# Optimization experiments

Hardware: AMD Instinct MI355X
Metric: run time of the kernel (lower is better)

## Reference

```python
import jax, jax.numpy as jnp
import numpy as np
import math

B, N, M, C, H = 8, 2048, 2048, 512, 8
DK = C // H
EPS_LN = 1e-5


def _layernorm(x, g, b):
    mu = jnp.mean(x, axis=-1, keepdims=True)
    var = jnp.var(x, axis=-1, keepdims=True)
    return (x - mu) / jnp.sqrt(var + EPS_LN) * g + b


def setup_inputs() -> dict:
    key = jax.random.key(0)
    ks = jax.random.split(key, 8)
    s = 0.02
    return {
        "cross_x": jax.random.normal(ks[0], (B, N, C), jnp.float32),
        "cross_y": jax.random.normal(ks[1], (B, M, C), jnp.float32),
        "ln_x_g": jnp.ones((C,), jnp.float32),
        "ln_x_b": jnp.zeros((C,), jnp.float32),
        "ln_y_g": jnp.ones((C,), jnp.float32),
        "ln_y_b": jnp.zeros((C,), jnp.float32),
        "Wq": jax.random.normal(ks[2], (C, C), jnp.float32) * s,
        "bq": jnp.zeros((C,), jnp.float32),
        "Wk": jax.random.normal(ks[3], (C, C), jnp.float32) * s,
        "bk": jnp.zeros((C,), jnp.float32),
        "Wv": jax.random.normal(ks[4], (C, C), jnp.float32) * s,
        "bv": jnp.zeros((C,), jnp.float32),
        "Wc": jax.random.normal(ks[5], (C, C), jnp.float32) * s,  # conv1x1 weight [out, in]
        "bc": jnp.zeros((C,), jnp.float32),
        "ln_o_g": jnp.ones((C,), jnp.float32),
        "ln_o_b": jnp.zeros((C,), jnp.float32),
    }


def reference(cross_x, cross_y, ln_x_g, ln_x_b, ln_y_g, ln_y_b,
              Wq, bq, Wk, bk, Wv, bv, Wc, bc, ln_o_g, ln_o_b):
    b, n, c = cross_x.shape
    m = cross_y.shape[1]
    xn = _layernorm(cross_x, ln_x_g, ln_x_b)
    yn = _layernorm(cross_y, ln_y_g, ln_y_b)
    # projections -> [B, H, seq, dk]
    q = (xn @ Wq + bq).reshape(b, n, H, DK).transpose(0, 2, 1, 3)
    k = (yn @ Wk + bk).reshape(b, m, H, DK).transpose(0, 2, 1, 3)
    v = (yn @ Wv + bv).reshape(b, m, H, DK).transpose(0, 2, 1, 3)
    scale = 1.0 / math.sqrt(DK)
    scores = jnp.einsum("bhnd,bhmd->bhnm", q, k) * scale
    attn = jax.nn.softmax(scores, axis=-1)
    # extra renormalization across the HEAD dimension (dim=1)
    attn = attn / (1e-9 + jnp.sum(attn, axis=1, keepdims=True))
    # dropout is identity in eval/reference mode
    o = jnp.einsum("bhnm,bhmd->bhnd", attn, v)
    q_flat = q.transpose(0, 2, 1, 3).reshape(b, n, c)  # [B, N, C]
    o_flat = o.transpose(0, 2, 1, 3).reshape(b, n, c)
    # conv1x1 over channels on (query - x)
    h = (q_flat - o_flat) @ Wc.T + bc
    h = jax.nn.leaky_relu(_layernorm(h, ln_o_g, ln_o_b), negative_slope=0.02)
    return q_flat + h
```

## Files before the change

kernel.cpp:

```cpp
#include <hip/hip_runtime.h>


typedef short bf16x8 __attribute__((ext_vector_type(8)));
typedef float f32x4 __attribute__((ext_vector_type(4)));

#define CS 0.18033688f

#define BARRIER_LG() do { __builtin_amdgcn_sched_barrier(0); \
  asm volatile("s_waitcnt lgkmcnt(0)" ::: "memory"); \
  __builtin_amdgcn_s_barrier(); \
  __builtin_amdgcn_sched_barrier(0); } while(0)

#define VMCNT(N) do { __builtin_amdgcn_sched_barrier(0); \
  asm volatile("s_waitcnt vmcnt(" #N ")" ::: "memory"); \
  __builtin_amdgcn_sched_barrier(0); } while(0)

__device__ inline float b2f(unsigned short u){
  union { unsigned int i; float f; } c; c.i = ((unsigned int)u) << 16; return c.f;
}
__device__ inline unsigned short f2b(float f){
  union { float ff; unsigned int i; } c; c.ff = f;
  unsigned int i = c.i;
  return (unsigned short)((i + 0x7FFFu + ((i >> 16) & 1u)) >> 16);
}
__device__ inline float fast_rcp(float x){ return __builtin_amdgcn_rcpf(x); }
__device__ inline f32x4 mfma16(bf16x8 a, bf16x8 b, f32x4 c){
  return __builtin_amdgcn_mfma_f32_16x16x32_bf16(a, b, c, 0, 0, 0);
}
__device__ __forceinline__ void gl16(const unsigned short* g, unsigned short* l){
  __builtin_amdgcn_global_load_lds(
      (const __attribute__((address_space(1))) unsigned int*)g,
      (__attribute__((address_space(3))) unsigned int*)l,
      16, 0, 0);
}

__global__ void detect_dtype(const unsigned int* __restrict__ g, int* __restrict__ flag){
  *flag = (g[0] == 0x3F800000u) ? 1 : 0;
}

__global__ void zero_f32(float* __restrict__ p, int n){
  int i = blockIdx.x * 256 + threadIdx.x;
  if (i < n) p[i] = 0.0f;
}

__global__ void convert_misc(const void* Wc, const void* bq, const void* bk,
    const void* bv, const void* bc, const void* go, const void* bo,
    unsigned short* WcB, unsigned short* bqB, unsigned short* bkB,
    unsigned short* bvB, unsigned short* bcB, unsigned short* goB,
    unsigned short* boB, const int* __restrict__ flag){
  int i = blockIdx.x * 256 + threadIdx.x;
  const void* src; unsigned short* dst; int o;
  if (i < 262144){ src = Wc; dst = WcB; o = i; }
  else {
    int j = i - 262144; int seg = j >> 9; o = j & 511;
    if (seg == 0){ src = bq; dst = bqB; }
    else if (seg == 1){ src = bk; dst = bkB; }
    else if (seg == 2){ src = bv; dst = bvB; }
    else if (seg == 3){ src = bc; dst = bcB; }
    else if (seg == 4){ src = go; dst = goB; }
    else if (seg == 5){ src = bo; dst = boB; }
    else return;
  }
  if (*flag) dst[o] = f2b(((const float*)src)[o]);
  else       dst[o] = ((const unsigned short*)src)[o];
}

__global__ __launch_bounds__(128) void ln_rows(const void* __restrict__ xv,
    const void* __restrict__ gxv, const void* __restrict__ bxv,
    const void* __restrict__ yv, const void* __restrict__ gyv, const void* __restrict__ byv,
    unsigned short* __restrict__ outx, unsigned short* __restrict__ outy,
    const int* __restrict__ flag){
  int row = blockIdx.x & 16383;
  int sel = blockIdx.x >> 14;
  const void* src = sel ? yv : xv;
  const void* gv = sel ? gyv : gxv;
  const void* bv_ = sel ? byv : bxv;
  unsigned short* out = sel ? outy : outx;
  int t = threadIdx.x;
  float v0, v1, v2, v3, g0, g1, g2, g3, bb0, bb1, bb2, bb3;
  if (*flag){
    float4 xf = ((const float4*)((const float*)src + (size_t)row * 512))[t];
    v0 = xf.x; v1 = xf.y; v2 = xf.z; v3 = xf.w;
    float4 gf = ((const float4*)gv)[t];  g0 = gf.x; g1 = gf.y; g2 = gf.z; g3 = gf.w;
    float4 bf = ((const float4*)bv_)[t]; bb0 = bf.x; bb1 = bf.y; bb2 = bf.z; bb3 = bf.w;
  } else {
    ushort4 raw = ((const ushort4*)((const unsigned short*)src + (size_t)row * 512))[t];
    v0 = b2f(raw.x); v1 = b2f(raw.y); v2 = b2f(raw.z); v3 = b2f(raw.w);
    ushort4 gr = ((const ushort4*)gv)[t];  g0 = b2f(gr.x); g1 = b2f(gr.y); g2 = b2f(gr.z); g3 = b2f(gr.w);
    ushort4 br = ((const ushort4*)bv_)[t]; bb0 = b2f(br.x); bb1 = b2f(br.y); bb2 = b2f(br.z); bb3 = b2f(br.w);
  }
  float s = v0 + v1 + v2 + v3;
  float sq = v0*v0 + v1*v1 + v2*v2 + v3*v3;
  #pragma unroll
  for (int off = 32; off; off >>= 1){
    s += __shfl_down(s, off, 64);
    sq += __shfl_down(sq, off, 64);
  }
  __shared__ float red[4];
  if ((t & 63) == 0){ red[(t >> 6)*2] = s; red[(t >> 6)*2 + 1] = sq; }
  __syncthreads();
  s = red[0] + red[2]; sq = red[1] + red[3];
  float mu = s * (1.0f/512.0f);
  float rstd = rsqrtf(sq * (1.0f/512.0f) - mu*mu + 1e-5f);
  ushort4 o;
  o.x = f2b((v0 - mu)*rstd*g0 + bb0);
  o.y = f2b((v1 - mu)*rstd*g1 + bb1);
  o.z = f2b((v2 - mu)*rstd*g2 + bb2);
  o.w = f2b((v3 - mu)*rstd*g3 + bb3);
  ((ushort4*)(out + (size_t)row * 512))[t] = o;
}

__global__ __launch_bounds__(256) void transposeW(const void* __restrict__ wq,
    const void* __restrict__ wk, const void* __restrict__ wv,
    unsigned short* __restrict__ oq, unsigned short* __restrict__ ok,
    unsigned short* __restrict__ ov, const int* __restrict__ flag){
  __shared__ unsigned short tile[32][33];
  const void* in = (blockIdx.z == 0) ? wq : (blockIdx.z == 1) ? wk : wv;
  unsigned short* outp = (blockIdx.z == 0) ? oq : (blockIdx.z == 1) ? ok : ov;
  int k0 = blockIdx.x * 32, j0 = blockIdx.y * 32;
  int t = threadIdx.x;
  int r = t >> 3, c4 = (t & 7) * 4;
  if (*flag){
    float4 v = *(const float4*)((const float*)in + (size_t)(k0 + r) * 512 + j0 + c4);
    tile[r][c4] = f2b(v.x); tile[r][c4+1] = f2b(v.y);
    tile[r][c4+2] = f2b(v.z); tile[r][c4+3] = f2b(v.w);
  } else {
    ushort4 v = *(const ushort4*)((const unsigned short*)in + (size_t)(k0 + r) * 512 + j0 + c4);
    tile[r][c4] = v.x; tile[r][c4+1] = v.y; tile[r][c4+2] = v.z; tile[r][c4+3] = v.w;
  }
  __syncthreads();
  ushort4 o;
  o.x = tile[c4][r]; o.y = tile[c4+1][r]; o.z = tile[c4+2][r]; o.w = tile[c4+3][r];
  *(ushort4*)(outp + (size_t)(j0 + r) * 512 + k0 + c4) = o;
}

template<int OUT_MODE>
__global__ __launch_bounds__(256) void gemm_nt(const unsigned short* __restrict__ A,
    const unsigned short* __restrict__ Bt, const unsigned short* __restrict__ bias,
    void* __restrict__ Cout){
  __shared__ __align__(16) unsigned short As[128*32];
  __shared__ __align__(16) unsigned short Bs[128*32];
  int i0 = blockIdx.x * 128;
  int j0 = blockIdx.y * 128;
  int t = threadIdx.x;
  int w = t >> 6, lane = t & 63;
  int quad = lane >> 4, l15 = lane & 15;
  int wrow = (w >> 1) * 64, wcol = (w & 1) * 64;
  f32x4 acc[4][4];
  #pragma unroll
  for (int a = 0; a < 4; a++)
    #pragma unroll
    for (int b = 0; b < 4; b++)
      acc[a][b] = (f32x4){0.f, 0.f, 0.f, 0.f};

  int ra0 = t >> 2, ca0 = (t & 3) * 8;
  const unsigned short* Ag = A + (size_t)i0 * 512;
  const unsigned short* Bg = Bt + (size_t)j0 * 512;

  for (int kt = 0; kt < 16; kt++){
    int k0 = kt * 32;
    int4 av0 = *(const int4*)(Ag + (size_t)ra0 * 512 + k0 + ca0);
    int4 av1 = *(const int4*)(Ag + (size_t)(64 + ra0) * 512 + k0 + ca0);
    int4 bv0 = *(const int4*)(Bg + (size_t)ra0 * 512 + k0 + ca0);
    int4 bv1 = *(const int4*)(Bg + (size_t)(64 + ra0) * 512 + k0 + ca0);
    __syncthreads();
    ((int4*)As)[t] = av0; ((int4*)As)[t + 256] = av1;
    ((int4*)Bs)[t] = bv0; ((int4*)Bs)[t + 256] = bv1;
    __syncthreads();
    bf16x8 af[4], bfg[4];
    #pragma unroll
    for (int a = 0; a < 4; a++)
      af[a] = *(const bf16x8*)&As[(wrow + a*16 + l15)*32 + quad*8];
    #pragma unroll
    for (int b = 0; b < 4; b++)
      bfg[b] = *(const bf16x8*)&Bs[(wcol + b*16 + l15)*32 + quad*8];
    #pragma unroll
    for (int a = 0; a < 4; a++)
      #pragma unroll
      for (int b = 0; b < 4; b++)
        acc[a][b] = mfma16(af[a], bfg[b], acc[a][b]);
  }

  #pragma unroll
  for (int b = 0; b < 4; b++){
    int gcol = j0 + wcol + b*16 + l15;
    float bv = b2f(bias[gcol]);
    #pragma unroll
    for (int a = 0; a < 4; a++){
      #pragma unroll
      for (int r = 0; r < 4; r++){
        int grow = i0 + wrow + a*16 + quad*4 + r;
        float v = acc[a][b][r] + bv;
        if (OUT_MODE == 0){
          ((unsigned short*)Cout)[(size_t)grow*512 + gcol] = f2b(v);
        } else {
          int bb_ = grow >> 11, m = grow & 2047;
          int h = gcol >> 6, d = gcol & 63;
          ((unsigned short*)Cout)[((size_t)((bb_*8 + h)*64 + d))*2048 + m] = f2b(v);
        }
      }
    }
  }
}

__global__ __launch_bounds__(256) void attn_lsum(const unsigned short* __restrict__ Qm,
    const unsigned short* __restrict__ Km, float* __restrict__ Lsum){
  int wgl = blockIdx.x * 4 + (threadIdx.x >> 6);
  int b = wgl >> 9; int r_ = wgl & 511;
  int ntl = r_ >> 4; int ms = (r_ >> 2) & 3; int hg = r_ & 3;
  int h0 = hg * 2;
  int lane = threadIdx.x & 63, quad = lane >> 4, l15 = lane & 15;
  int n0 = ntl * 64;
  const unsigned short* Kp = Km + ((size_t)(b*2048)) * 512;
  bf16x8 aq[4][2][2];
  #pragma unroll
  for (int ns = 0; ns < 4; ns++)
    #pragma unroll
    for (int hh = 0; hh < 2; hh++)
      #pragma unroll
      for (int ks = 0; ks < 2; ks++)
        aq[ns][hh][ks] = *(const bf16x8*)(Qm + ((size_t)(b*2048 + n0 + ns*16 + l15))*512
                                          + (h0+hh)*64 + ks*32 + quad*8);
  float ls[4][2];
  #pragma unroll
  for (int ns = 0; ns < 4; ns++){ ls[ns][0] = 0.f; ls[ns][1] = 0.f; }
  for (int mt = 0; mt < 16; mt++){
    int m0 = ms*512 + mt*32;
    #pragma unroll
    for (int msub = 0; msub < 2; msub++){
      int mb = m0 + msub*16;
      #pragma unroll
      for (int hh = 0; hh < 2; hh++){
        bf16x8 ak0 = *(const bf16x8*)(Kp + (size_t)(mb + l15)*512 + (h0+hh)*64 + quad*8);
        bf16x8 ak1 = *(const bf16x8*)(Kp + (size_t)(mb + l15)*512 + (h0+hh)*64 + 32 + quad*8);
        #pragma unroll
        for (int ns = 0; ns < 4; ns++){
          f32x4 S = (f32x4){0.f,0.f,0.f,0.f};
          S = mfma16(ak0, aq[ns][hh][0], S);
          S = mfma16(ak1, aq[ns][hh][1], S);
          float e0 = exp2f(S[0]*CS), e1 = exp2f(S[1]*CS);
          float e2 = exp2f(S[2]*CS), e3 = exp2f(S[3]*CS);
          ls[ns][hh] += (e0 + e1) + (e2 + e3);
        }
      }
    }
  }
  #pragma unroll
  for (int ns = 0; ns < 4; ns++)
    #pragma unroll
    for (int hh = 0; hh < 2; hh++){
      float v = ls[ns][hh];
      v += __shfl_xor(v, 16, 64);
      v += __shfl_xor(v, 32, 64);
      ls[ns][hh] = v;
    }
  if (lane < 16){
    #pragma unroll
    for (int ns = 0; ns < 4; ns++)
      #pragma unroll
      for (int hh = 0; hh < 2; hh++)
        atomicAdd(&Lsum[(size_t)(b*8 + h0 + hh)*2048 + n0 + ns*16 + lane], ls[ns][hh]);
  }
}

__global__ __launch_bounds__(1024, 4) void attn_out(const unsigned short* __restrict__ Qm,
    const unsigned short* __restrict__ Km, const unsigned short* __restrict__ VTm,
    const float* __restrict__ Lsum, unsigned short* __restrict__ DQO){
  __shared__ __align__(16) unsigned short Ks[32*512];
  __shared__ __align__(16) unsigned short Vs[512*32];
  __shared__ __align__(16) float ps[4*4*16*36];
  __shared__ __align__(16) unsigned short pbv[4*4*2*16*40];
  int bid = blockIdx.x;
  int b = bid & 7;
  int ntl = bid >> 3;
  int t = threadIdx.x;
  int w = t >> 6;
  int hp = w & 3;
  int nsub = w >> 2;
  int lane = t & 63, quad = lane >> 4, l15 = lane & 15;
  int h0 = hp * 2;
  int n0 = ntl * 64 + nsub * 16;
  int kx = (l15 & 7) << 4;

  const unsigned short* Kg = Km + (size_t)b * 1048576;
  const unsigned short* Vg = VTm + (size_t)b * 1048576;
  const unsigned short* Qp = Qm + ((size_t)(b*2048 + n0)) * 512;

  bf16x8 aq[2][2];
  #pragma unroll
  for (int hh = 0; hh < 2; hh++)
    #pragma unroll
    for (int ks = 0; ks < 2; ks++)
      aq[hh][ks] = *(const bf16x8*)(Qp + (size_t)l15*512 + (h0+hh)*64 + ks*32 + quad*8);
  float lg[2];
  #pragma unroll
  for (int hh = 0; hh < 2; hh++)
    lg[hh] = -log2f(Lsum[(size_t)(b*8 + h0 + hh)*2048 + n0 + l15]);
  f32x4 oacc[2][4];
  #pragma unroll
  for (int hh = 0; hh < 2; hh++)
    #pragma unroll
    for (int d = 0; d < 4; d++)
      oacc[hh][d] = (f32x4){0.f,0.f,0.f,0.f};

  int ksl = (lane ^ (w & 7)) << 3;
  int vro = (lane >> 2), vco = (lane & 3) * 8;
  unsigned short* kd0 = Ks + (w << 9);
  unsigned short* kd1 = Ks + ((w + 16) << 9);
  unsigned short* vd0 = Vs + (w << 9);
  unsigned short* vd1 = Vs + ((w + 16) << 9);

  float* psn = ps + nsub * 2304;
  float* pso = psn + hp * 576 + l15 * 36;
  unsigned short* pbn = pbv + nsub * 5120 + hp * 1280;

  gl16(Kg + ((size_t)(w     ) << 9) + ksl, kd0);
  gl16(Kg + ((size_t)(w + 16) << 9) + ksl, kd1);
  gl16(Vg + ((size_t)( w*16       + vro) << 11) + vco, vd0);
  gl16(Vg + ((size_t)((w+16)*16   + vro) << 11) + vco, vd1);

  for (int mt = 0; mt < 64; mt++){
    VMCNT(2);
    BARRIER_LG();
    float p[2][2][4];
    f32x4 s_own[2];
    #pragma unroll
    for (int msub = 0; msub < 2; msub++){
      const char* kr = (const char*)Ks + ((msub*16 + l15) << 10);
      #pragma unroll
      for (int hh = 0; hh < 2; hh++){
        int cb = (h0 + hh) * 128;
        bf16x8 k0 = *(const bf16x8*)(kr + ((cb + quad*16) ^ kx));
        bf16x8 k1 = *(const bf16x8*)(kr + ((cb + 64 + quad*16) ^ kx));
        f32x4 S = (f32x4){0.f,0.f,0.f,0.f};
        S = mfma16(k0, aq[hh][0], S);
        S = mfma16(k1, aq[hh][1], S);
        #pragma unroll
        for (int r = 0; r < 4; r++) p[hh][msub][r] = exp2f(fmaf(S[r], CS, lg[hh]));
      }
      f32x4 so;
      #pragma unroll
      for (int r = 0; r < 4; r++) so[r] = p[0][msub][r] + p[1][msub][r];
      s_own[msub] = so;
      *(f32x4*)(pso + msub*16 + quad*4) = so;
    }
    VMCNT(0);
    BARRIER_LG();
    if (mt < 63){
      const unsigned short* Kt = Kg + ((size_t)(mt+1) << 14);
      gl16(Kt + ((size_t)(w     ) << 9) + ksl, kd0);
      gl16(Kt + ((size_t)(w + 16) << 9) + ksl, kd1);
    }
    f32x4 ir4[2];
    #pragma unroll
    for (int msub = 0; msub < 2; msub++){
      f32x4 tt = s_own[msub];
      #pragma unroll
      for (int j = 1; j < 4; j++){
        int hq = (hp + j) & 3;
        tt += *(const f32x4*)(psn + hq*576 + l15*36 + msub*16 + quad*4);
      }
      f32x4 ir;
      #pragma unroll
      for (int r = 0; r < 4; r++) ir[r] = fast_rcp(1e-9f + tt[r]);
      ir4[msub] = ir;
    }
    #pragma unroll
    for (int hh = 0; hh < 2; hh++){
      #pragma unroll
      for (int msub = 0; msub < 2; msub++){
        unsigned int lo = (unsigned int)f2b(p[hh][msub][0]*ir4[msub][0])
                        | ((unsigned int)f2b(p[hh][msub][1]*ir4[msub][1]) << 16);
        unsigned int hi = (unsigned int)f2b(p[hh][msub][2]*ir4[msub][2])
                        | ((unsigned int)f2b(p[hh][msub][3]*ir4[msub][3]) << 16);
        int2 pv; pv.x = (int)lo; pv.y = (int)hi;
        *(int2*)&pbn[(hh*16 + l15)*40 + msub*16 + quad*4] = pv;
      }
    }
    #pragma unroll
    for (int hh = 0; hh < 2; hh++){
      bf16x8 wp = *(const bf16x8*)((const char*)pbn + (hh*16 + l15)*80 + quad*16);
      const char* vb = (const char*)Vs + (((h0+hh)*64 + l15) << 6) + quad*16;
      #pragma unroll
      for (int d = 0; d < 4; d++){
        bf16x8 vv = *(const bf16x8*)(vb + (d << 10));
        oacc[hh][d] = mfma16(vv, wp, oacc[hh][d]);
      }
    }
    BARRIER_LG();
    if (mt < 63){
      int m1 = (mt + 1) * 32;
      gl16(Vg + ((size_t)( w*16     + vro) << 11) + m1 + vco, vd0);
      gl16(Vg + ((size_t)((w+16)*16 + vro) << 11) + m1 + vco, vd1);
    }
  }
  {
    size_t nrow = (size_t)(b*2048 + n0 + l15);
    const unsigned short* Qrow = Qm + nrow * 512;
    unsigned short* Drow = DQO + nrow * 512;
    #pragma unroll
    for (int hh = 0; hh < 2; hh++){
      #pragma unroll
      for (int d = 0; d < 4; d++){
        int c = (h0+hh)*64 + d*16 + quad*4;
        ushort4 qv = *(const ushort4*)(Qrow + c);
        ushort4 ov;
        ov.x = f2b(b2f(qv.x) - oacc[hh][d][0]);
        ov.y = f2b(b2f(qv.y) - oacc[hh][d][1]);
        ov.z = f2b(b2f(qv.z) - oacc[hh][d][2]);
        ov.w = f2b(b2f(qv.w) - oacc[hh][d][3]);
        *(ushort4*)(Drow + c) = ov;
      }
    }
  }
}

__global__ __launch_bounds__(128) void finalize_k(const unsigned short* __restrict__ H,
    const unsigned short* __restrict__ Qb, const unsigned short* __restrict__ g,
    const unsigned short* __restrict__ bb, void* __restrict__ outp,
    const int* __restrict__ flag){
  int row = blockIdx.x; int t = threadIdx.x;
  ushort4 hraw = ((const ushort4*)(H + (size_t)row * 512))[t];
  float h0 = b2f(hraw.x), h1 = b2f(hraw.y), h2 = b2f(hraw.z), h3 = b2f(hraw.w);
  float s = h0 + h1 + h2 + h3;
  float sq = h0*h0 + h1*h1 + h2*h2 + h3*h3;
  #pragma unroll
  for (int off = 32; off; off >>= 1){
    s += __shfl_down(s, off, 64);
    sq += __shfl_down(sq, off, 64);
  }
  __shared__ float red[4];
  if ((t & 63) == 0){ red[(t >> 6)*2] = s; red[(t >> 6)*2 + 1] = sq; }
  __syncthreads();
  s = red[0] + red[2]; sq = red[1] + red[3];
  float mu = s * (1.0f/512.0f);
  float rstd = rsqrtf(sq * (1.0f/512.0f) - mu*mu + 1e-5f);
  ushort4 gr = ((const ushort4*)g)[t];
  ushort4 br = ((const ushort4*)bb)[t];
  ushort4 qr = ((const ushort4*)(Qb + (size_t)row * 512))[t];
  float y0 = (h0 - mu)*rstd*b2f(gr.x) + b2f(br.x); y0 = fmaxf(y0, 0.02f*y0);
  float y1 = (h1 - mu)*rstd*b2f(gr.y) + b2f(br.y); y1 = fmaxf(y1, 0.02f*y1);
  float y2 = (h2 - mu)*rstd*b2f(gr.z) + b2f(br.z); y2 = fmaxf(y2, 0.02f*y2);
  float y3 = (h3 - mu)*rstd*b2f(gr.w) + b2f(br.w); y3 = fmaxf(y3, 0.02f*y3);
  float o0 = b2f(qr.x) + y0, o1 = b2f(qr.y) + y1, o2 = b2f(qr.z) + y2, o3 = b2f(qr.w) + y3;
  if (*flag){
    float4 o; o.x = o0; o.y = o1; o.z = o2; o.w = o3;
    ((float4*)((float*)outp + (size_t)row * 512))[t] = o;
  } else {
    ushort4 o; o.x = f2b(o0); o.y = f2b(o1); o.z = f2b(o2); o.w = f2b(o3);
    ((ushort4*)((unsigned short*)outp + (size_t)row * 512))[t] = o;
  }
}

extern "C" void kernel_launch(void* const* d_in, const int* in_sizes, int n_in,
                              void* d_out, int out_size, void* d_ws, size_t ws_size,
                              hipStream_t stream){
  const void* x      = d_in[0];
  const void* y      = d_in[1];
  const void* ln_x_g = d_in[2];
  const void* ln_x_b = d_in[3];
  const void* ln_y_g = d_in[4];
  const void* ln_y_b = d_in[5];
  const void* Wq     = d_in[6];
  const void* bq     = d_in[7];
  const void* Wk     = d_in[8];
  const void* bk     = d_in[9];
  const void* Wv     = d_in[10];
  const void* bv     = d_in[11];
  const void* Wc     = d_in[12];
  const void* bc     = d_in[13];
  const void* ln_o_g = d_in[14];
  const void* ln_o_b = d_in[15];

  const size_t MB = (size_t)1 << 20;
  char* ws = (char*)d_ws;
  unsigned short* Qb  = (unsigned short*)(ws);
  unsigned short* Kb  = (unsigned short*)(ws + 16*MB);
  unsigned short* VT  = (unsigned short*)(ws + 32*MB);
  unsigned short* XN  = (unsigned short*)(ws + 48*MB);
  unsigned short* YN  = (unsigned short*)(ws + 64*MB);
  unsigned short* DQO = XN;
  unsigned short* Hpre = YN;
  unsigned short* WqT = (unsigned short*)(ws + 80*MB);
  unsigned short* WkT = WqT + 512*512;
  unsigned short* WvT = WkT + 512*512;
  unsigned short* WcB = WvT + 512*512;
  unsigned short* bqB = (unsigned short*)(ws + 82*MB);
  unsigned short* bkB = bqB + 512;
  unsigned short* bvB = bkB + 512;
  unsigned short* bcB = bvB + 512;
  unsigned short* goB = bcB + 512;
  unsigned short* boB = goB + 512;
  float* Lsum         = (float*)(ws + 83*MB);
  int* Flag           = (int*)(ws + 84*MB);

  detect_dtype<<<dim3(1), dim3(1), 0, stream>>>((const unsigned int*)ln_x_g, Flag);
  zero_f32<<<dim3(512), dim3(256), 0, stream>>>(Lsum, 131072);
  convert_misc<<<dim3(1037), dim3(256), 0, stream>>>(Wc, bq, bk, bv, bc, ln_o_g, ln_o_b,
      WcB, bqB, bkB, bvB, bcB, goB, boB, Flag);
  ln_rows<<<dim3(32768), dim3(128), 0, stream>>>(x, ln_x_g, ln_x_b, y, ln_y_g, ln_y_b,
      XN, YN, Flag);
  transposeW<<<dim3(16,16,3), dim3(256), 0, stream>>>(Wq, Wk, Wv, WqT, WkT, WvT, Flag);
  gemm_nt<0><<<dim3(128,4), dim3(256), 0, stream>>>(XN, WqT, bqB, (void*)Qb);
  gemm_nt<0><<<dim3(128,4), dim3(256), 0, stream>>>(YN, WkT, bkB, (void*)Kb);
  gemm_nt<2><<<dim3(128,4), dim3(256), 0, stream>>>(YN, WvT, bvB, (void*)VT);
  attn_lsum<<<dim3(1024), dim3(256), 0, stream>>>(Qb, Kb, Lsum);
  attn_out<<<dim3(256), dim3(1024), 0, stream>>>(Qb, Kb, VT, Lsum, DQO);
  gemm_nt<0><<<dim3(128,4), dim3(256), 0, stream>>>(DQO, WcB, bcB, (void*)Hpre);
  finalize_k<<<dim3(16384), dim3(128), 0, stream>>>(Hpre, Qb, goB, boB, d_out, Flag);
}
```

Measured before the change: 525.2 us.

## Load V fragments directly to registers with tiled layout, drop V LDS staging

The V projection output is written in an m-tiled layout (32-row chunks), so each wave can fetch its bf16x8 V fragments straight from global memory into registers instead of staging the V tile through LDS. The per-tile V LDS buffer, the trailing barrier and the separate V async copies go away, and vmcnt waits are reworked so register V loads for the next tile overlap the current PV MFMAs. P-to-bf16 packing also switches to the hardware v_cvt_pk_bf16_f32 instruction. In exchange, the same V data is now read from global memory by the four waves that share a head pair (different query sub-tiles) rather than once into shared LDS, more registers are used, and the vmcnt counting must line up with the mixed LDS and register loads.

```diff
diff --git a/kernel.cpp b/kernel.cpp
--- a/kernel.cpp
+++ b/kernel.cpp
@@ -22,6 +22,11 @@
   union { float ff; unsigned int i; } c; c.ff = f;
   unsigned int i = c.i;
   return (unsigned short)((i + 0x7FFFu + ((i >> 16) & 1u)) >> 16);
+}
+__device__ inline unsigned int cvtpk(float lo, float hi){
+  unsigned int r;
+  asm("v_cvt_pk_bf16_f32 %0, %1, %2" : "=v"(r) : "v"(lo), "v"(hi));
+  return r;
 }
 __device__ inline float fast_rcp(float x){ return __builtin_amdgcn_rcpf(x); }
 __device__ inline f32x4 mfma16(bf16x8 a, bf16x8 b, f32x4 c){
@@ -196,7 +201,8 @@
         } else {
           int bb_ = grow >> 11, m = grow & 2047;
           int h = gcol >> 6, d = gcol & 63;
-          ((unsigned short*)Cout)[((size_t)((bb_*8 + h)*64 + d))*2048 + m] = f2b(v);
+          ((unsigned short*)Cout)[(((size_t)(bb_*64 + (m >> 5))*512) + h*64 + d)*32
+                                  + (m & 31)] = f2b(v);
         }
       }
     }
@@ -267,7 +273,6 @@
     const unsigned short* __restrict__ Km, const unsigned short* __restrict__ VTm,
     const float* __restrict__ Lsum, unsigned short* __restrict__ DQO){
   __shared__ __align__(16) unsigned short Ks[32*512];
-  __shared__ __align__(16) unsigned short Vs[512*32];
   __shared__ __align__(16) float ps[4*4*16*36];
   __shared__ __align__(16) unsigned short pbv[4*4*2*16*40];
   int bid = blockIdx.x;
@@ -283,7 +288,6 @@
   int kx = (l15 & 7) << 4;
 
   const unsigned short* Kg = Km + (size_t)b * 1048576;
-  const unsigned short* Vg = VTm + (size_t)b * 1048576;
   const unsigned short* Qp = Qm + ((size_t)(b*2048 + n0)) * 512;
 
   bf16x8 aq[2][2];
@@ -304,23 +308,28 @@
       oacc[hh][d] = (f32x4){0.f,0.f,0.f,0.f};
 
   int ksl = (lane ^ (w & 7)) << 3;
-  int vro = (lane >> 2), vco = (lane & 3) * 8;
   unsigned short* kd0 = Ks + (w << 9);
   unsigned short* kd1 = Ks + ((w + 16) << 9);
-  unsigned short* vd0 = Vs + (w << 9);
-  unsigned short* vd1 = Vs + ((w + 16) << 9);
 
   float* psn = ps + nsub * 2304;
   float* pso = psn + hp * 576 + l15 * 36;
   unsigned short* pbn = pbv + nsub * 5120 + hp * 1280;
 
-  gl16(Kg + ((size_t)(w     ) << 9) + ksl, kd0);
+  const unsigned short* vb0 = VTm + (size_t)b*1048576 + (h0*64 + l15)*32 + quad*8;
+  const unsigned short* vb1 = vb0 + 64*32;
+
+  gl16(Kg + ((size_t)w << 9) + ksl, kd0);
   gl16(Kg + ((size_t)(w + 16) << 9) + ksl, kd1);
-  gl16(Vg + ((size_t)( w*16       + vro) << 11) + vco, vd0);
-  gl16(Vg + ((size_t)((w+16)*16   + vro) << 11) + vco, vd1);
+  bf16x8 vf[2][4];
+  #pragma unroll
+  for (int d = 0; d < 4; d++){
+    vf[0][d] = *(const bf16x8*)(vb0 + d*512);
+    vf[1][d] = *(const bf16x8*)(vb1 + d*512);
+  }
+  vb0 += 16384; vb1 += 16384;
 
   for (int mt = 0; mt < 64; mt++){
-    VMCNT(2);
+    VMCNT(8);
     BARRIER_LG();
     float p[2][2][4];
     f32x4 s_own[2];
@@ -344,11 +353,10 @@
       s_own[msub] = so;
       *(f32x4*)(pso + msub*16 + quad*4) = so;
     }
-    VMCNT(0);
     BARRIER_LG();
     if (mt < 63){
       const unsigned short* Kt = Kg + ((size_t)(mt+1) << 14);
-      gl16(Kt + ((size_t)(w     ) << 9) + ksl, kd0);
+      gl16(Kt + ((size_t)w << 9) + ksl, kd0);
       gl16(Kt + ((size_t)(w + 16) << 9) + ksl, kd1);
     }
     f32x4 ir4[2];
@@ -369,29 +377,28 @@
     for (int hh = 0; hh < 2; hh++){
       #pragma unroll
       for (int msub = 0; msub < 2; msub++){
-        unsigned int lo = (unsigned int)f2b(p[hh][msub][0]*ir4[msub][0])
-                        | ((unsigned int)f2b(p[hh][msub][1]*ir4[msub][1]) << 16);
-        unsigned int hi = (unsigned int)f2b(p[hh][msub][2]*ir4[msub][2])
-                        | ((unsigned int)f2b(p[hh][msub][3]*ir4[msub][3]) << 16);
-        int2 pv; pv.x = (int)lo; pv.y = (int)hi;
+        int2 pv;
+        pv.x = (int)cvtpk(p[hh][msub][0]*ir4[msub][0], p[hh][msub][1]*ir4[msub][1]);
+        pv.y = (int)cvtpk(p[hh][msub][2]*ir4[msub][2], p[hh][msub][3]*ir4[msub][3]);
         *(int2*)&pbn[(hh*16 + l15)*40 + msub*16 + quad*4] = pv;
       }
     }
+    if (mt < 63) { VMCNT(2); }
+    else         { VMCNT(0); }
     #pragma unroll
     for (int hh = 0; hh < 2; hh++){
       bf16x8 wp = *(const bf16x8*)((const char*)pbn + (hh*16 + l15)*80 + quad*16);
-      const char* vb = (const char*)Vs + (((h0+hh)*64 + l15) << 6) + quad*16;
+      #pragma unroll
+      for (int d = 0; d < 4; d++)
+        oacc[hh][d] = mfma16(vf[hh][d], wp, oacc[hh][d]);
+    }
+    if (mt < 63){
       #pragma unroll
       for (int d = 0; d < 4; d++){
-        bf16x8 vv = *(const bf16x8*)(vb + (d << 10));
-        oacc[hh][d] = mfma16(vv, wp, oacc[hh][d]);
-      }
-    }
-    BARRIER_LG();
-    if (mt < 63){
-      int m1 = (mt + 1) * 32;
-      gl16(Vg + ((size_t)( w*16     + vro) << 11) + m1 + vco, vd0);
-      gl16(Vg + ((size_t)((w+16)*16 + vro) << 11) + m1 + vco, vd1);
+        vf[0][d] = *(const bf16x8*)(vb0 + d*512);
+        vf[1][d] = *(const bf16x8*)(vb1 + d*512);
+      }
+      vb0 += 16384; vb1 += 16384;
     }
   }
   {
```

After: 602.9 us. +14.8%, slower.

## Tile V^T layout by 32-key blocks for contiguous loads; use packed bf16 convert

Applied to the files above, without the earlier changes.

The V projection now writes V^T in a blocked layout where each group of 32 keys for all heads and dims is contiguous. The attention kernel can then fetch each V tile as one linear 32 KB chunk instead of strided 64-byte row pieces, which should improve memory coalescing. The per-element software bf16 rounding of probabilities is replaced with the hardware v_cvt_pk_bf16_f32 instruction. The launch bounds are changed to use the amdgpu_waves_per_eu attribute. The GEMM epilogue store now scatters differently, which may change its write efficiency.

```diff
diff --git a/kernel.cpp b/kernel.cpp
--- a/kernel.cpp
+++ b/kernel.cpp
@@ -22,6 +22,11 @@
   union { float ff; unsigned int i; } c; c.ff = f;
   unsigned int i = c.i;
   return (unsigned short)((i + 0x7FFFu + ((i >> 16) & 1u)) >> 16);
+}
+__device__ inline unsigned int cvtpk(float lo, float hi){
+  unsigned int r;
+  asm("v_cvt_pk_bf16_f32 %0, %1, %2" : "=v"(r) : "v"(lo), "v"(hi));
+  return r;
 }
 __device__ inline float fast_rcp(float x){ return __builtin_amdgcn_rcpf(x); }
 __device__ inline f32x4 mfma16(bf16x8 a, bf16x8 b, f32x4 c){
@@ -196,7 +201,8 @@
         } else {
           int bb_ = grow >> 11, m = grow & 2047;
           int h = gcol >> 6, d = gcol & 63;
-          ((unsigned short*)Cout)[((size_t)((bb_*8 + h)*64 + d))*2048 + m] = f2b(v);
+          ((unsigned short*)Cout)[(((size_t)(bb_*64 + (m >> 5))*512) + h*64 + d)*32
+                                  + (m & 31)] = f2b(v);
         }
       }
     }
@@ -263,7 +269,9 @@
   }
 }
 
-__global__ __launch_bounds__(1024, 4) void attn_out(const unsigned short* __restrict__ Qm,
+__global__ __launch_bounds__(1024)
+__attribute__((amdgpu_waves_per_eu(4, 4)))
+void attn_out(const unsigned short* __restrict__ Qm,
     const unsigned short* __restrict__ Km, const unsigned short* __restrict__ VTm,
     const float* __restrict__ Lsum, unsigned short* __restrict__ DQO){
   __shared__ __align__(16) unsigned short Ks[32*512];
@@ -304,11 +312,10 @@
       oacc[hh][d] = (f32x4){0.f,0.f,0.f,0.f};
 
   int ksl = (lane ^ (w & 7)) << 3;
-  int vro = (lane >> 2), vco = (lane & 3) * 8;
   unsigned short* kd0 = Ks + (w << 9);
   unsigned short* kd1 = Ks + ((w + 16) << 9);
-  unsigned short* vd0 = Vs + (w << 9);
-  unsigned short* vd1 = Vs + ((w + 16) << 9);
+  unsigned short* vd0 = Vs + t*8;
+  unsigned short* vd1 = Vs + t*8 + 8192;
 
   float* psn = ps + nsub * 2304;
   float* pso = psn + hp * 576 + l15 * 36;
@@ -316,8 +323,8 @@
 
   gl16(Kg + ((size_t)(w     ) << 9) + ksl, kd0);
   gl16(Kg + ((size_t)(w + 16) << 9) + ksl, kd1);
-  gl16(Vg + ((size_t)( w*16       + vro) << 11) + vco, vd0);
-  gl16(Vg + ((size_t)((w+16)*16   + vro) << 11) + vco, vd1);
+  gl16(Vg + t*8, vd0);
+  gl16(Vg + t*8 + 8192, vd1);
 
   for (int mt = 0; mt < 64; mt++){
     VMCNT(2);
@@ -369,11 +376,9 @@
     for (int hh = 0; hh < 2; hh++){
       #pragma unroll
       for (int msub = 0; msub < 2; msub++){
-        unsigned int lo = (unsigned int)f2b(p[hh][msub][0]*ir4[msub][0])
-                        | ((unsigned int)f2b(p[hh][msub][1]*ir4[msub][1]) << 16);
-        unsigned int hi = (unsigned int)f2b(p[hh][msub][2]*ir4[msub][2])
-                        | ((unsigned int)f2b(p[hh][msub][3]*ir4[msub][3]) << 16);
-        int2 pv; pv.x = (int)lo; pv.y = (int)hi;
+        int2 pv;
+        pv.x = (int)cvtpk(p[hh][msub][0]*ir4[msub][0], p[hh][msub][1]*ir4[msub][1]);
+        pv.y = (int)cvtpk(p[hh][msub][2]*ir4[msub][2], p[hh][msub][3]*ir4[msub][3]);
         *(int2*)&pbn[(hh*16 + l15)*40 + msub*16 + quad*4] = pv;
       }
     }
@@ -389,9 +394,9 @@
     }
     BARRIER_LG();
     if (mt < 63){
-      int m1 = (mt + 1) * 32;
-      gl16(Vg + ((size_t)( w*16     + vro) << 11) + m1 + vco, vd0);
-      gl16(Vg + ((size_t)((w+16)*16 + vro) << 11) + m1 + vco, vd1);
+      const unsigned short* Vt = Vg + ((size_t)(mt+1) << 14);
+      gl16(Vt + t*8, vd0);
+      gl16(Vt + t*8 + 8192, vd1);
     }
   }
   {
```

New measurement: 525.0 us. About the same (-0.0%).
